# Kernel tuning notes

Measured on AMD Instinct MI355X. Metric: run time of the kernel, lower is better.

Reference implementation:

```python
import jax, jax.numpy as jnp
import numpy as np

B, S, D, H = 4, 1024, 1024, 16
HD = D // H  # head_dim = 64


def setup_inputs() -> dict:
    key = jax.random.key(0)
    ks = jax.random.split(key, 12)
    std = 1.0 / np.sqrt(D)
    inp = {
        "query": jax.random.normal(ks[0], (B, S, D), jnp.float32),
        "key": jax.random.normal(ks[1], (B, S, D), jnp.float32),
        "value": jax.random.normal(ks[2], (B, S, D), jnp.float32),
        # four Linear(embed_dim, embed_dim) layers: q, k, v, out
        "Wq": jax.random.normal(ks[3], (D, D), jnp.float32) * std,
        "bq": jnp.zeros((D,), jnp.float32),
        "Wk": jax.random.normal(ks[4], (D, D), jnp.float32) * std,
        "bk": jnp.zeros((D,), jnp.float32),
        "Wv": jax.random.normal(ks[5], (D, D), jnp.float32) * std,
        "bv": jnp.zeros((D,), jnp.float32),
        "Wo": jax.random.normal(ks[6], (D, D), jnp.float32) * std,
        "bo": jnp.zeros((D,), jnp.float32),
        # compressor: Linear(num_heads, 1)
        "Wc": jax.random.normal(ks[7], (H,), jnp.float32) / np.sqrt(H),
        "bc": jnp.zeros((), jnp.float32),
    }
    return inp


def reference(query, key, value, Wq, bq, Wk, bk, Wv, bv, Wo, bo, Wc, bc):
    b, s, d = query.shape
    h, hd = H, HD

    def proj(x, W, bias):
        # [b,s,d] @ [d,d] -> [b,h,s,hd]
        y = jnp.einsum('bsd,de->bse', x, W) + bias
        return y.reshape(b, s, h, hd).transpose(0, 2, 1, 3)

    q = proj(query, Wq, bq)
    k = proj(key, Wk, bk)
    v = proj(value, Wv, bv)

    scores = jnp.einsum('bhqd,bhkd->bhqk', q, k) / np.sqrt(hd)
    p_attn = jax.nn.softmax(scores, axis=-1)  # [b,h,s,s]; dropout is identity in eval

    x = jnp.einsum('bhqk,bhkd->bhqd', p_attn, v)
    x = x.transpose(0, 2, 1, 3).reshape(b, s, d)
    out = jnp.einsum('bsd,de->bse', x, Wo) + bo

    # head compression: Linear(num_heads, 1) over head axis -> [b,1,s,s]
    attn_c = (jnp.einsum('bhqk,h->bqk', p_attn, Wc) + bc)[:, None, :, :]
    return out, attn_c
```

## Files before the change

### kernel.cpp

```cpp
#include <hip/hip_runtime.h>
#include <hip/hip_bf16.h>

#define SS 1024
#define DD 1024
#define HH 16
#define HDh 64

typedef short bf16x8 __attribute__((ext_vector_type(8)));
typedef float f32x4 __attribute__((ext_vector_type(4)));

__device__ inline unsigned short f2bf(float f) {
    union { __hip_bfloat16 h; unsigned short u; } cv;
    cv.h = __float2bfloat16(f);
    return cv.u;
}
__device__ inline float bf2f(short u) {
    unsigned int x = ((unsigned int)(unsigned short)u) << 16;
    return __uint_as_float(x);
}

#define PIN4(a, b, c, d) asm volatile("" : "+v"(a), "+v"(b), "+v"(c), "+v"(d))

__device__ inline void gload_lds16(const unsigned short* g, unsigned short* l) {
    __builtin_amdgcn_global_load_lds(
        (const __attribute__((address_space(1))) unsigned int*)g,
        (__attribute__((address_space(3))) unsigned int*)l, 16, 0, 0);
}

__global__ __launch_bounds__(256) void prep(
    const float* __restrict__ a, const float* __restrict__ b, const float* __restrict__ c,
    unsigned short* __restrict__ oa, unsigned short* __restrict__ ob, unsigned short* __restrict__ oc,
    const float* __restrict__ Wq, const float* __restrict__ Wk,
    const float* __restrict__ Wv, const float* __restrict__ Wo,
    unsigned short* __restrict__ oq, unsigned short* __restrict__ okk,
    unsigned short* __restrict__ ov, unsigned short* __restrict__ oo)
{
    __shared__ float tile[32][33];
    int bid = blockIdx.x;
    if (bid < 4096) {
        size_t i = ((size_t)bid * 256 + threadIdx.x) * 4;
        float4 va = *(const float4*)(a + i);
        float4 vb = *(const float4*)(b + i);
        float4 vc = *(const float4*)(c + i);
        *(ushort4*)(oa + i) = make_ushort4(f2bf(va.x), f2bf(va.y), f2bf(va.z), f2bf(va.w));
        *(ushort4*)(ob + i) = make_ushort4(f2bf(vb.x), f2bf(vb.y), f2bf(vb.z), f2bf(vb.w));
        *(ushort4*)(oc + i) = make_ushort4(f2bf(vc.x), f2bf(vc.y), f2bf(vc.z), f2bf(vc.w));
    } else {
        int idx = bid - 4096;
        int z = idx >> 10;
        const float* W = z == 0 ? Wq : (z == 1 ? Wk : (z == 2 ? Wv : Wo));
        unsigned short* O = z == 0 ? oq : (z == 1 ? okk : (z == 2 ? ov : oo));
        int e0 = (idx & 31) * 32, d0 = ((idx >> 5) & 31) * 32;
        int r = threadIdx.x >> 3, c4 = (threadIdx.x & 7) * 4;
        float4 v = *(const float4*)(W + (size_t)(d0 + r) * DD + e0 + c4);
        tile[r][c4 + 0] = v.x; tile[r][c4 + 1] = v.y; tile[r][c4 + 2] = v.z; tile[r][c4 + 3] = v.w;
        __syncthreads();
        ushort4 u = make_ushort4(f2bf(tile[c4 + 0][r]), f2bf(tile[c4 + 1][r]),
                                 f2bf(tile[c4 + 2][r]), f2bf(tile[c4 + 3][r]));
        *(ushort4*)(O + (size_t)(e0 + r) * DD + d0 + c4) = u;
    }
}

template<int BK>
__device__ inline void gemm128_core(const unsigned short* __restrict__ A,
                                    const unsigned short* __restrict__ Bt,
                                    const float* __restrict__ bias,
                                    void* __restrict__ out, int mode, float oscale,
                                    int m0, int n0)
{
    __shared__ unsigned short As[128 * BK];
    __shared__ unsigned short Bs[128 * BK];
    int t = threadIdx.x;
    int w = t >> 6, lane = t & 63, quad = lane >> 4, l15 = lane & 15;
    int wm = w >> 1, wn = w & 1;

    f32x4 zero = {0.f, 0.f, 0.f, 0.f};
    f32x4 acc[4][4];
#pragma unroll
    for (int i = 0; i < 4; i++)
#pragma unroll
        for (int j = 0; j < 4; j++) acc[i][j] = zero;

    for (int k0 = 0; k0 < DD; k0 += BK) {
        __syncthreads();
        if constexpr (BK == 32) {
#pragma unroll
            for (int i = 0; i < 4; i++) {
                int chunk = w + i * 4;
                int half = chunk >> 3;
                int c = chunk & 7;
                const unsigned short* g = (half ? Bt : A)
                    + (size_t)((half ? n0 : m0) + c * 16 + (lane >> 2)) * DD + k0 + (lane & 3) * 8;
                unsigned short* l = (half ? Bs : As) + c * 512 + lane * 8;
                gload_lds16(g, l);
            }
        } else {
#pragma unroll
            for (int i = 0; i < 8; i++) {
                int chunk = w + i * 4;
                int half = chunk >> 4;
                int sub = chunk & 15;
                const unsigned short* g = (half ? Bt : A)
                    + (size_t)((half ? n0 : m0) + (sub >> 1) * 16 + (lane >> 2)) * DD
                    + k0 + (sub & 1) * 32 + (lane & 3) * 8;
                unsigned short* l = (half ? Bs : As) + sub * 512 + lane * 8;
                gload_lds16(g, l);
            }
        }
        __syncthreads();
        if constexpr (BK == 32) {
            bf16x8 af[4], bfr[4];
#pragma unroll
            for (int mi = 0; mi < 4; mi++)
                af[mi] = *(const bf16x8*)&As[(wm * 64 + mi * 16 + l15) * 32 + quad * 8];
#pragma unroll
            for (int ni = 0; ni < 4; ni++)
                bfr[ni] = *(const bf16x8*)&Bs[(wn * 64 + ni * 16 + l15) * 32 + quad * 8];
#pragma unroll
            for (int mi = 0; mi < 4; mi++)
#pragma unroll
                for (int ni = 0; ni < 4; ni++)
                    acc[mi][ni] = __builtin_amdgcn_mfma_f32_16x16x32_bf16(af[mi], bfr[ni], acc[mi][ni], 0, 0, 0);
        } else {
#pragma unroll
            for (int kk = 0; kk < 2; kk++) {
                bf16x8 af[4], bfr[4];
#pragma unroll
                for (int mi = 0; mi < 4; mi++)
                    af[mi] = *(const bf16x8*)&As[((wm * 4 + mi) * 2 + kk) * 512 + l15 * 32 + quad * 8];
#pragma unroll
                for (int ni = 0; ni < 4; ni++)
                    bfr[ni] = *(const bf16x8*)&Bs[((wn * 4 + ni) * 2 + kk) * 512 + l15 * 32 + quad * 8];
#pragma unroll
                for (int mi = 0; mi < 4; mi++)
#pragma unroll
                    for (int ni = 0; ni < 4; ni++)
                        acc[mi][ni] = __builtin_amdgcn_mfma_f32_16x16x32_bf16(af[mi], bfr[ni], acc[mi][ni], 0, 0, 0);
            }
        }
    }

#pragma unroll
    for (int mi = 0; mi < 4; mi++)
#pragma unroll
        for (int ni = 0; ni < 4; ni++) {
            int n = n0 + wn * 64 + ni * 16 + l15;
            float bv = bias[n];
#pragma unroll
            for (int r = 0; r < 4; r++) {
                int m = m0 + wm * 64 + mi * 16 + quad * 4 + r;
                float v = (acc[mi][ni][r] + bv) * oscale;
                if (mode == 2) {
                    ((float*)out)[(size_t)m * DD + n] = v;
                } else {
                    int bb = m >> 10, s = m & 1023, hh = n >> 6, d = n & 63;
                    size_t head = (size_t)(bb * HH + hh) << 16;
                    size_t off;
                    if (mode == 0) {
                        off = head + (((size_t)(s >> 4) * 2 + (d >> 5)) * 64
                              + ((d >> 3) & 3) * 16 + (s & 15)) * 8 + (d & 7);
                    } else {
                        off = head + (((size_t)(s >> 5) * 4 + (d >> 4)) * 64
                              + ((s >> 3) & 3) * 16 + (d & 15)) * 8 + (s & 7);
                    }
                    ((unsigned short*)out)[off] = f2bf(v);
                }
            }
        }
}

#define SCLQ 0.18033688f

__global__ __launch_bounds__(256, 3) void gemm_qkv(
    const unsigned short* __restrict__ xq, const unsigned short* __restrict__ xk,
    const unsigned short* __restrict__ xv,
    const unsigned short* __restrict__ wtq, const unsigned short* __restrict__ wtk,
    const unsigned short* __restrict__ wtv,
    const float* __restrict__ bq, const float* __restrict__ bk, const float* __restrict__ bv,
    unsigned short* __restrict__ q, unsigned short* __restrict__ k, unsigned short* __restrict__ v)
{
    int bid = blockIdx.x;
    int swz = (bid & 7) * 96 + (bid >> 3);
    int z = swz >> 8, rem = swz & 255;
    int n0 = (rem & 7) * 128, m0 = (rem >> 3) * 128;
    const unsigned short* A  = z == 0 ? xq  : (z == 1 ? xk  : xv);
    const unsigned short* Bt = z == 0 ? wtq : (z == 1 ? wtk : wtv);
    const float* bias        = z == 0 ? bq  : (z == 1 ? bk  : bv);
    void* out                = z == 0 ? (void*)q : (z == 1 ? (void*)k : (void*)v);
    gemm128_core<64>(A, Bt, bias, out, z == 2 ? 1 : 0, z == 0 ? SCLQ : 1.0f, m0, n0);
}

__global__ __launch_bounds__(256, 3) void gemm_o(
    const unsigned short* __restrict__ x, const unsigned short* __restrict__ wto,
    const float* __restrict__ bo, float* __restrict__ out)
{
    int bid = blockIdx.x;
    int swz = (bid & 7) * 32 + (bid >> 3);
    int n0 = (swz & 7) * 128, m0 = (swz >> 3) * 128;
    gemm128_core<32>(x, wto, bo, out, 2, 1.0f, m0, n0);
}


__global__ __launch_bounds__(512, 4) void fattn_kernel(
    const unsigned short* __restrict__ qf, const unsigned short* __restrict__ kf,
    const unsigned short* __restrict__ vf, float* __restrict__ Z,
    unsigned short* __restrict__ xat)
{
    __shared__ __align__(16) unsigned short kls[2][2048];
    __shared__ __align__(16) unsigned short vls[2][2048];
    __shared__ __align__(16) unsigned short plds[8][640];
    int t = threadIdx.x, w = t >> 6, lane = t & 63, quad = lane >> 4, l15 = lane & 15;
    int bid = blockIdx.x;
    int swz = (bid & 7) * 64 + (bid >> 3);
    int bh = swz >> 3, m0 = (swz & 7) * 128;
    int b = bh >> 4, h = bh & 15;
    const unsigned short* qh = qf + ((size_t)bh << 16);
    const unsigned short* kh = kf + ((size_t)bh << 16);
    const unsigned short* vh = vf + ((size_t)bh << 16);

    bf16x8 qfrag[2];
    int s16b = (m0 >> 4) + w;
#pragma unroll
    for (int dh = 0; dh < 2; dh++)
        qfrag[dh] = *(const bf16x8*)(qh + (size_t)(s16b * 2 + dh) * 512 + lane * 8);

    f32x4 zero = {0.f, 0.f, 0.f, 0.f};
    f32x4 oacc[4];
#pragma unroll
    for (int ni = 0; ni < 4; ni++) oacc[ni] = zero;
    float zacc = 0.f;

    const unsigned short* ssrc = (w < 4 ? kh + (size_t)w * 512
                                        : vh + (size_t)(w - 4) * 512) + lane * 8;
    int sinner = (w < 4 ? w * 512 : (w - 4) * 512) + lane * 8;

    gload_lds16(ssrc, (w < 4 ? kls[0] : vls[0]) + sinner);
    __syncthreads();

    int cur = 0;
    for (int kt = 0; kt < 32; kt++) {
        if (kt < 31)
            gload_lds16(ssrc + (size_t)(kt + 1) * 2048,
                        (w < 4 ? kls[cur ^ 1] : vls[cur ^ 1]) + sinner);

        bf16x8 kc[4], vc[4];
#pragma unroll
        for (int i = 0; i < 4; i++) {
            kc[i] = *(const bf16x8*)&kls[cur][i * 512 + lane * 8];
            vc[i] = *(const bf16x8*)&vls[cur][i * 512 + lane * 8];
        }

        f32x4 st[2];
#pragma unroll
        for (int si = 0; si < 2; si++) {
            st[si] = __builtin_amdgcn_mfma_f32_16x16x32_bf16(kc[si * 2 + 0], qfrag[0], zero, 0, 0, 0);
            st[si] = __builtin_amdgcn_mfma_f32_16x16x32_bf16(kc[si * 2 + 1], qfrag[1], st[si], 0, 0, 0);
        }

#pragma unroll
        for (int si = 0; si < 2; si++) {
            float p0 = exp2f(st[si][0]);
            float p1 = exp2f(st[si][1]);
            float p2 = exp2f(st[si][2]);
            float p3 = exp2f(st[si][3]);
            zacc += (p0 + p1) + (p2 + p3);
            unsigned int pk0 = (unsigned int)f2bf(p0) | ((unsigned int)f2bf(p1) << 16);
            unsigned int pk1 = (unsigned int)f2bf(p2) | ((unsigned int)f2bf(p3) << 16);
            *(uint2*)&plds[w][l15 * 40 + si * 16 + quad * 4] = make_uint2(pk0, pk1);
        }
        bf16x8 pa = *(const bf16x8*)&plds[w][l15 * 40 + quad * 8];

#pragma unroll
        for (int ni = 0; ni < 4; ni++)
            oacc[ni] = __builtin_amdgcn_mfma_f32_16x16x32_bf16(pa, vc[ni], oacc[ni], 0, 0, 0);

        __syncthreads();
        cur ^= 1;
    }

    float zt = zacc;
    zt += __shfl_xor(zt, 16);
    zt += __shfl_xor(zt, 32);
    if (quad == 0)
        Z[(size_t)bh * 1024 + m0 + w * 16 + l15] = zt;

#pragma unroll
    for (int r = 0; r < 4; r++) {
        int qrow = quad * 4 + r;
        float iz = 1.f / __shfl(zt, qrow);
        int q = m0 + w * 16 + qrow;
#pragma unroll
        for (int ni = 0; ni < 4; ni++)
            xat[((size_t)(b * 1024 + q)) * 1024 + h * 64 + ni * 16 + l15] =
                f2bf(oacc[ni][r] * iz);
    }
}

__global__ __launch_bounds__(256, 3) void tail_kernel(
    const unsigned short* __restrict__ qf, const unsigned short* __restrict__ kf,
    const float* __restrict__ Z, const float* __restrict__ Wc,
    const float* __restrict__ bcp, float* __restrict__ attc,
    const unsigned short* __restrict__ xat, const unsigned short* __restrict__ wto,
    const float* __restrict__ bo, float* __restrict__ out0)
{
    if (blockIdx.x >= 512) {
        int bid2 = blockIdx.x - 512;
        int swz = (bid2 & 7) * 32 + (bid2 >> 3);
        int n0 = (swz & 7) * 128, m0 = (swz >> 3) * 128;
        gemm128_core<32>(xat, wto, bo, out0, 2, 1.0f, m0, n0);
        return;
    }
    __shared__ unsigned short ks[2][8192];
    int t = threadIdx.x, w = t >> 6, lane = t & 63, quad = lane >> 4, l15 = lane & 15;
    int bid = blockIdx.x;
    int u = (bid & 7) * 64 + (bid >> 3);
    int kb = u & 7, qg = (u >> 3) & 15, b = u >> 7;
    int qt = qg * 4 + w;
    int q = qt * 16 + l15;
    float bc = *bcp;
    f32x4 zero = {0.f, 0.f, 0.f, 0.f};
    f32x4 acc[4][2];
#pragma unroll
    for (int kt = 0; kt < 4; kt++)
#pragma unroll
        for (int si = 0; si < 2; si++) acc[kt][si] = zero;

    float wzv[16];
#pragma unroll
    for (int h = 0; h < 16; h++)
        wzv[h] = Wc[h] / Z[(size_t)(b * 16 + h) * 1024 + q];

    {
        const unsigned short* src = kf + ((size_t)(b * 16) << 16) + (size_t)(kb * 16) * 512;
#pragma unroll
        for (int i = 0; i < 4; i++) {
            int c = w + i * 4;
            gload_lds16(src + (size_t)c * 512 + lane * 8, ks[0] + c * 512 + lane * 8);
        }
    }
    __syncthreads();

    int cb = 0;
    for (int h = 0; h < 16; h++) {
        int bh = b * 16 + h;
        const unsigned short* qh = qf + ((size_t)bh << 16);
        bf16x8 qfr0 = *(const bf16x8*)(qh + (size_t)(qt * 2 + 0) * 512 + lane * 8);
        bf16x8 qfr1 = *(const bf16x8*)(qh + (size_t)(qt * 2 + 1) * 512 + lane * 8);
        if (h < 15) {
            const unsigned short* src = kf + ((size_t)(bh + 1) << 16) + (size_t)(kb * 16) * 512;
#pragma unroll
            for (int i = 0; i < 4; i++) {
                int c = w + i * 4;
                gload_lds16(src + (size_t)c * 512 + lane * 8, ks[cb ^ 1] + c * 512 + lane * 8);
            }
        }
        float wz = wzv[h];
#pragma unroll
        for (int kt = 0; kt < 4; kt++) {
            bf16x8 kfr[4];
#pragma unroll
            for (int i = 0; i < 4; i++)
                kfr[i] = *(const bf16x8*)&ks[cb][(size_t)(kt * 4 + i) * 512 + lane * 8];
#pragma unroll
            for (int si = 0; si < 2; si++) {
                f32x4 st = __builtin_amdgcn_mfma_f32_16x16x32_bf16(kfr[si * 2 + 0], qfr0, zero, 0, 0, 0);
                st = __builtin_amdgcn_mfma_f32_16x16x32_bf16(kfr[si * 2 + 1], qfr1, st, 0, 0, 0);
#pragma unroll
                for (int r = 0; r < 4; r++)
                    acc[kt][si][r] += wz * exp2f(st[r]);
            }
        }
        __syncthreads();
        cb ^= 1;
    }
#pragma unroll
    for (int kt = 0; kt < 4; kt++)
#pragma unroll
        for (int si = 0; si < 2; si++) {
            float4 vv = make_float4(acc[kt][si][0] + bc, acc[kt][si][1] + bc,
                                    acc[kt][si][2] + bc, acc[kt][si][3] + bc);
            *(float4*)(attc + ((size_t)(b * 1024 + q)) * 1024 + kb * 128 + kt * 32 + si * 16 + quad * 4) = vv;
        }
}

#define LDK(f) (*(const bf16x8*)(kh + ((size_t)(f) * 64 + lane) * 8))
#define LDV(f) (*(const bf16x8*)(vh + ((size_t)(f) * 64 + lane) * 8))

__global__ __launch_bounds__(1024, 4) void attn_kernel(
    const unsigned short* __restrict__ qf, const unsigned short* __restrict__ kf,
    const unsigned short* __restrict__ vf, const float* __restrict__ Wc,
    const float* __restrict__ bcp, unsigned short* __restrict__ xout,
    float* __restrict__ attc)
{
    __shared__ float accc[16][1028];
    __shared__ unsigned short tsc[16][16][36];

    int t = threadIdx.x, w = t >> 6, lane = t & 63, quad = lane >> 4, l15 = lane & 15;
    int b = blockIdx.x >> 6, qt = blockIdx.x & 63;
    int h = w;

    for (int i = t; i < 16 * 1028; i += 1024) (&accc[0][0])[i] = 0.f;
    __syncthreads();

    const unsigned short* qh = qf + ((size_t)(b * HH + h) << 16);
    const unsigned short* kh = kf + ((size_t)(b * HH + h) << 16);
    const unsigned short* vh = vf + ((size_t)(b * HH + h) << 16);
    float wc = Wc[h], bc = *bcp;
    f32x4 zero = {0.f, 0.f, 0.f, 0.f};

    bf16x8 a0 = *(const bf16x8*)(qh + ((size_t)(qt * 2 + 0) * 64 + lane) * 8);
    bf16x8 a1 = *(const bf16x8*)(qh + ((size_t)(qt * 2 + 1) * 64 + lane) * 8);

    float rs[4] = {0.f, 0.f, 0.f, 0.f};
    bf16x8 c0 = LDK(0), c1 = LDK(1), c2 = LDK(2), c3 = LDK(3);
    PIN4(c0, c1, c2, c3);
    bf16x8 d0 = LDK(4), d1 = LDK(5), d2 = LDK(6), d3 = LDK(7);
    PIN4(d0, d1, d2, d3);
#pragma unroll 2
    for (int g = 0; g < 32; g++) {
        int gn = g < 30 ? g + 2 : 31;
        bf16x8 n0 = LDK(gn * 4 + 0), n1 = LDK(gn * 4 + 1);
        bf16x8 n2 = LDK(gn * 4 + 2), n3 = LDK(gn * 4 + 3);
        PIN4(n0, n1, n2, n3);
        f32x4 s0 = zero, s1 = zero;
        s0 = __builtin_amdgcn_mfma_f32_16x16x32_bf16(a0, c0, s0, 0, 0, 0);
        s0 = __builtin_amdgcn_mfma_f32_16x16x32_bf16(a1, c1, s0, 0, 0, 0);
        s1 = __builtin_amdgcn_mfma_f32_16x16x32_bf16(a0, c2, s1, 0, 0, 0);
        s1 = __builtin_amdgcn_mfma_f32_16x16x32_bf16(a1, c3, s1, 0, 0, 0);
#pragma unroll
        for (int r = 0; r < 4; r++) rs[r] += exp2f(s0[r]) + exp2f(s1[r]);
        c0 = d0; c1 = d1; c2 = d2; c3 = d3;
        d0 = n0; d1 = n1; d2 = n2; d3 = n3;
    }
#pragma unroll
    for (int r = 0; r < 4; r++) {
        rs[r] += __shfl_xor(rs[r], 1);
        rs[r] += __shfl_xor(rs[r], 2);
        rs[r] += __shfl_xor(rs[r], 4);
        rs[r] += __shfl_xor(rs[r], 8);
    }
    float invC[4], sC[4];
#pragma unroll
    for (int r = 0; r < 4; r++) { invC[r] = 1.f / rs[r]; sC[r] = wc * invC[r]; }

    f32x4 o0 = zero, o1 = zero, o2 = zero, o3 = zero;
    int cc0 = (2 * w) & 31;
    bf16x8 k0 = LDK(cc0 * 4 + 0), k1 = LDK(cc0 * 4 + 1);
    bf16x8 k2 = LDK(cc0 * 4 + 2), k3 = LDK(cc0 * 4 + 3);
    PIN4(k0, k1, k2, k3);
    bf16x8 v0 = LDV(cc0 * 4 + 0), v1 = LDV(cc0 * 4 + 1);
    bf16x8 v2 = LDV(cc0 * 4 + 2), v3 = LDV(cc0 * 4 + 3);
    PIN4(v0, v1, v2, v3);
#pragma unroll 2
    for (int i = 0; i < 32; i++) {
        int cc = (i + 2 * w) & 31;
        int cn = ((i + 1) + 2 * w) & 31;
        bf16x8 kn0 = LDK(cn * 4 + 0), kn1 = LDK(cn * 4 + 1);
        bf16x8 kn2 = LDK(cn * 4 + 2), kn3 = LDK(cn * 4 + 3);
        PIN4(kn0, kn1, kn2, kn3);
        bf16x8 vn0 = LDV(cn * 4 + 0), vn1 = LDV(cn * 4 + 1);
        bf16x8 vn2 = LDV(cn * 4 + 2), vn3 = LDV(cn * 4 + 3);
        PIN4(vn0, vn1, vn2, vn3);

        f32x4 s0 = zero, s1 = zero;
        s0 = __builtin_amdgcn_mfma_f32_16x16x32_bf16(a0, k0, s0, 0, 0, 0);
        s0 = __builtin_amdgcn_mfma_f32_16x16x32_bf16(a1, k1, s0, 0, 0, 0);
        s1 = __builtin_amdgcn_mfma_f32_16x16x32_bf16(a0, k2, s1, 0, 0, 0);
        s1 = __builtin_amdgcn_mfma_f32_16x16x32_bf16(a1, k3, s1, 0, 0, 0);

#pragma unroll
        for (int r = 0; r < 4; r++) {
            float p0 = exp2f(s0[r]);
            float p1 = exp2f(s1[r]);
            int row = quad * 4 + r;
            tsc[w][row][l15] = f2bf(p0);
            tsc[w][row][16 + l15] = f2bf(p1);
            atomicAdd(&accc[row][cc * 32 + l15], sC[r] * p0);
            atomicAdd(&accc[row][cc * 32 + 16 + l15], sC[r] * p1);
        }
        bf16x8 ap = *(const bf16x8*)&tsc[w][l15][quad * 8];

        o0 = __builtin_amdgcn_mfma_f32_16x16x32_bf16(ap, v0, o0, 0, 0, 0);
        o1 = __builtin_amdgcn_mfma_f32_16x16x32_bf16(ap, v1, o1, 0, 0, 0);
        o2 = __builtin_amdgcn_mfma_f32_16x16x32_bf16(ap, v2, o2, 0, 0, 0);
        o3 = __builtin_amdgcn_mfma_f32_16x16x32_bf16(ap, v3, o3, 0, 0, 0);
        k0 = kn0; k1 = kn1; k2 = kn2; k3 = kn3;
        v0 = vn0; v1 = vn1; v2 = vn2; v3 = vn3;
    }

    f32x4 oo[4] = {o0, o1, o2, o3};
#pragma unroll
    for (int j = 0; j < 4; j++)
#pragma unroll
        for (int r = 0; r < 4; r++) {
            int row = quad * 4 + r;
            xout[((size_t)(b * SS) + qt * 16 + row) * DD + h * 64 + j * 16 + l15] =
                f2bf(oo[j][r] * invC[r]);
        }

    __syncthreads();
    for (int i = t; i < 16 * 1024; i += 1024) {
        int row = i >> 10, col = i & 1023;
        attc[((size_t)b * SS + qt * 16 + row) * SS + col] = accc[row][col] + bc;
    }
}

extern "C" void kernel_launch(void* const* d_in, const int* in_sizes, int n_in,
                              void* d_out, int out_size, void* d_ws, size_t ws_size,
                              hipStream_t stream) {
    const float* query = (const float*)d_in[0];
    const float* key   = (const float*)d_in[1];
    const float* value = (const float*)d_in[2];
    const float* Wq = (const float*)d_in[3];
    const float* bq = (const float*)d_in[4];
    const float* Wk = (const float*)d_in[5];
    const float* bk = (const float*)d_in[6];
    const float* Wv = (const float*)d_in[7];
    const float* bv = (const float*)d_in[8];
    const float* Wo = (const float*)d_in[9];
    const float* bo = (const float*)d_in[10];
    const float* Wc = (const float*)d_in[11];
    const float* bc = (const float*)d_in[12];

    unsigned short* ws  = (unsigned short*)d_ws;
    unsigned short* xq  = ws;
    unsigned short* xk  = xq  + (size_t)4194304;
    unsigned short* xv  = xk  + (size_t)4194304;
    unsigned short* wtq = xv  + (size_t)4194304;
    unsigned short* wtk = wtq + (size_t)1048576;
    unsigned short* wtv = wtk + (size_t)1048576;
    unsigned short* wto = wtv + (size_t)1048576;
    unsigned short* qfb = wto + (size_t)1048576;
    unsigned short* kfb = qfb + (size_t)4194304;
    unsigned short* vfb = kfb + (size_t)4194304;
    unsigned short* xat = vfb + (size_t)4194304;

    float* out0 = (float*)d_out;
    float* attc = out0 + (size_t)4194304;

    const size_t base_bytes = 67108864;
    const size_t z_bytes = 262144;
    bool fast = ws_size >= base_bytes + z_bytes;

    hipLaunchKernelGGL(prep, dim3(8192), dim3(256), 0, stream,
                       query, key, value, xq, xk, xv,
                       Wq, Wk, Wv, Wo, wtq, wtk, wtv, wto);
    hipLaunchKernelGGL(gemm_qkv, dim3(768), dim3(256), 0, stream,
                       xq, xk, xv, wtq, wtk, wtv, bq, bk, bv, qfb, kfb, vfb);

    if (fast) {
        float* Zbuf = (float*)((char*)d_ws + base_bytes);
        hipLaunchKernelGGL(fattn_kernel, dim3(512), dim3(512), 0, stream,
                           qfb, kfb, vfb, Zbuf, xat);
        hipLaunchKernelGGL(tail_kernel, dim3(768), dim3(256), 0, stream,
                           qfb, kfb, Zbuf, Wc, bc, attc,
                           xat, wto, bo, out0);
    } else {
        hipLaunchKernelGGL(attn_kernel, dim3(256), dim3(1024), 0, stream,
                           qfb, kfb, vfb, Wc, bc, xat, attc);
        hipLaunchKernelGGL(gemm_o, dim3(256), dim3(256), 0, stream,
                           xat, wto, bo, out0);
    }
}
```

Before: 225.3 us.

## Double attention K/V tile depth, share LDS pool, use BK=64 for output GEMM

The flash-attention kernel now stages 64 keys per pipeline step instead of 32, so every wave loads both K and V chunks and two sub-tiles are processed per barrier, halving loop iterations and syncs. The GEMM core now takes caller-provided LDS buffers, and the tail kernel shares one pool between its compression path and its fused output-projection GEMM, which now runs with BK=64. The aim is to cut barrier and loop overhead and LDS over-allocation in the fused tail kernel. The cost is more LDS per attention block, which may lower occupancy.

```diff
diff --git a/kernel.cpp b/kernel.cpp
--- a/kernel.cpp
+++ b/kernel.cpp
@@ -62,14 +62,13 @@
 }
 
 template<int BK>
-__device__ inline void gemm128_core(const unsigned short* __restrict__ A,
+__device__ inline void gemm128_core(unsigned short* As, unsigned short* Bs,
+                                    const unsigned short* __restrict__ A,
                                     const unsigned short* __restrict__ Bt,
                                     const float* __restrict__ bias,
                                     void* __restrict__ out, int mode, float oscale,
                                     int m0, int n0)
 {
-    __shared__ unsigned short As[128 * BK];
-    __shared__ unsigned short Bs[128 * BK];
     int t = threadIdx.x;
     int w = t >> 6, lane = t & 63, quad = lane >> 4, l15 = lane & 15;
     int wm = w >> 1, wn = w & 1;
@@ -179,6 +178,7 @@
     const float* __restrict__ bq, const float* __restrict__ bk, const float* __restrict__ bv,
     unsigned short* __restrict__ q, unsigned short* __restrict__ k, unsigned short* __restrict__ v)
 {
+    __shared__ unsigned short pool[16384];
     int bid = blockIdx.x;
     int swz = (bid & 7) * 96 + (bid >> 3);
     int z = swz >> 8, rem = swz & 255;
@@ -187,17 +187,19 @@
     const unsigned short* Bt = z == 0 ? wtq : (z == 1 ? wtk : wtv);
     const float* bias        = z == 0 ? bq  : (z == 1 ? bk  : bv);
     void* out                = z == 0 ? (void*)q : (z == 1 ? (void*)k : (void*)v);
-    gemm128_core<64>(A, Bt, bias, out, z == 2 ? 1 : 0, z == 0 ? SCLQ : 1.0f, m0, n0);
+    gemm128_core<64>(pool, pool + 8192, A, Bt, bias, out, z == 2 ? 1 : 0,
+                     z == 0 ? SCLQ : 1.0f, m0, n0);
 }
 
 __global__ __launch_bounds__(256, 3) void gemm_o(
     const unsigned short* __restrict__ x, const unsigned short* __restrict__ wto,
     const float* __restrict__ bo, float* __restrict__ out)
 {
+    __shared__ unsigned short pool[16384];
     int bid = blockIdx.x;
     int swz = (bid & 7) * 32 + (bid >> 3);
     int n0 = (swz & 7) * 128, m0 = (swz >> 3) * 128;
-    gemm128_core<32>(x, wto, bo, out, 2, 1.0f, m0, n0);
+    gemm128_core<64>(pool, pool + 8192, x, wto, bo, out, 2, 1.0f, m0, n0);
 }
 
 
@@ -206,8 +208,8 @@
     const unsigned short* __restrict__ vf, float* __restrict__ Z,
     unsigned short* __restrict__ xat)
 {
-    __shared__ __align__(16) unsigned short kls[2][2048];
-    __shared__ __align__(16) unsigned short vls[2][2048];
+    __shared__ __align__(16) unsigned short kls[2][4096];
+    __shared__ __align__(16) unsigned short vls[2][4096];
     __shared__ __align__(16) unsigned short plds[8][640];
     int t = threadIdx.x, w = t >> 6, lane = t & 63, quad = lane >> 4, l15 = lane & 15;
     int bid = blockIdx.x;
@@ -230,49 +232,54 @@
     for (int ni = 0; ni < 4; ni++) oacc[ni] = zero;
     float zacc = 0.f;
 
-    const unsigned short* ssrc = (w < 4 ? kh + (size_t)w * 512
-                                        : vh + (size_t)(w - 4) * 512) + lane * 8;
-    int sinner = (w < 4 ? w * 512 : (w - 4) * 512) + lane * 8;
-
-    gload_lds16(ssrc, (w < 4 ? kls[0] : vls[0]) + sinner);
+    const unsigned short* ksrc = kh + (size_t)w * 512 + lane * 8;
+    const unsigned short* vsrc = vh + (size_t)w * 512 + lane * 8;
+    int koff = w * 512 + lane * 8;
+
+    gload_lds16(ksrc, kls[0] + koff);
+    gload_lds16(vsrc, vls[0] + koff);
     __syncthreads();
 
     int cur = 0;
-    for (int kt = 0; kt < 32; kt++) {
-        if (kt < 31)
-            gload_lds16(ssrc + (size_t)(kt + 1) * 2048,
-                        (w < 4 ? kls[cur ^ 1] : vls[cur ^ 1]) + sinner);
-
-        bf16x8 kc[4], vc[4];
-#pragma unroll
-        for (int i = 0; i < 4; i++) {
-            kc[i] = *(const bf16x8*)&kls[cur][i * 512 + lane * 8];
-            vc[i] = *(const bf16x8*)&vls[cur][i * 512 + lane * 8];
-        }
-
-        f32x4 st[2];
-#pragma unroll
-        for (int si = 0; si < 2; si++) {
-            st[si] = __builtin_amdgcn_mfma_f32_16x16x32_bf16(kc[si * 2 + 0], qfrag[0], zero, 0, 0, 0);
-            st[si] = __builtin_amdgcn_mfma_f32_16x16x32_bf16(kc[si * 2 + 1], qfrag[1], st[si], 0, 0, 0);
-        }
-
-#pragma unroll
-        for (int si = 0; si < 2; si++) {
-            float p0 = exp2f(st[si][0]);
-            float p1 = exp2f(st[si][1]);
-            float p2 = exp2f(st[si][2]);
-            float p3 = exp2f(st[si][3]);
-            zacc += (p0 + p1) + (p2 + p3);
-            unsigned int pk0 = (unsigned int)f2bf(p0) | ((unsigned int)f2bf(p1) << 16);
-            unsigned int pk1 = (unsigned int)f2bf(p2) | ((unsigned int)f2bf(p3) << 16);
-            *(uint2*)&plds[w][l15 * 40 + si * 16 + quad * 4] = make_uint2(pk0, pk1);
-        }
-        bf16x8 pa = *(const bf16x8*)&plds[w][l15 * 40 + quad * 8];
-
-#pragma unroll
-        for (int ni = 0; ni < 4; ni++)
-            oacc[ni] = __builtin_amdgcn_mfma_f32_16x16x32_bf16(pa, vc[ni], oacc[ni], 0, 0, 0);
+    for (int p = 0; p < 16; p++) {
+        if (p < 15) {
+            gload_lds16(ksrc + (size_t)(p + 1) * 4096, kls[cur ^ 1] + koff);
+            gload_lds16(vsrc + (size_t)(p + 1) * 4096, vls[cur ^ 1] + koff);
+        }
+
+#pragma unroll
+        for (int sub = 0; sub < 2; sub++) {
+            bf16x8 kc[4], vc[4];
+#pragma unroll
+            for (int i = 0; i < 4; i++) {
+                kc[i] = *(const bf16x8*)&kls[cur][(sub * 4 + i) * 512 + lane * 8];
+                vc[i] = *(const bf16x8*)&vls[cur][(sub * 4 + i) * 512 + lane * 8];
+            }
+
+            f32x4 st[2];
+#pragma unroll
+            for (int si = 0; si < 2; si++) {
+                st[si] = __builtin_amdgcn_mfma_f32_16x16x32_bf16(kc[si * 2 + 0], qfrag[0], zero, 0, 0, 0);
+                st[si] = __builtin_amdgcn_mfma_f32_16x16x32_bf16(kc[si * 2 + 1], qfrag[1], st[si], 0, 0, 0);
+            }
+
+#pragma unroll
+            for (int si = 0; si < 2; si++) {
+                float p0 = exp2f(st[si][0]);
+                float p1 = exp2f(st[si][1]);
+                float p2 = exp2f(st[si][2]);
+                float p3 = exp2f(st[si][3]);
+                zacc += (p0 + p1) + (p2 + p3);
+                unsigned int pk0 = (unsigned int)f2bf(p0) | ((unsigned int)f2bf(p1) << 16);
+                unsigned int pk1 = (unsigned int)f2bf(p2) | ((unsigned int)f2bf(p3) << 16);
+                *(uint2*)&plds[w][l15 * 40 + si * 16 + quad * 4] = make_uint2(pk0, pk1);
+            }
+            bf16x8 pa = *(const bf16x8*)&plds[w][l15 * 40 + quad * 8];
+
+#pragma unroll
+            for (int ni = 0; ni < 4; ni++)
+                oacc[ni] = __builtin_amdgcn_mfma_f32_16x16x32_bf16(pa, vc[ni], oacc[ni], 0, 0, 0);
+        }
 
         __syncthreads();
         cur ^= 1;
@@ -303,14 +310,16 @@
     const unsigned short* __restrict__ xat, const unsigned short* __restrict__ wto,
     const float* __restrict__ bo, float* __restrict__ out0)
 {
+    __shared__ __align__(16) unsigned short pool[16384];
     if (blockIdx.x >= 512) {
         int bid2 = blockIdx.x - 512;
         int swz = (bid2 & 7) * 32 + (bid2 >> 3);
         int n0 = (swz & 7) * 128, m0 = (swz >> 3) * 128;
-        gemm128_core<32>(xat, wto, bo, out0, 2, 1.0f, m0, n0);
+        gemm128_core<64>(pool, pool + 8192, xat, wto, bo, out0, 2, 1.0f, m0, n0);
         return;
     }
-    __shared__ unsigned short ks[2][8192];
+    unsigned short* ks0 = pool;
+    unsigned short* ks1 = pool + 8192;
     int t = threadIdx.x, w = t >> 6, lane = t & 63, quad = lane >> 4, l15 = lane & 15;
     int bid = blockIdx.x;
     int u = (bid & 7) * 64 + (bid >> 3);
@@ -335,7 +344,7 @@
 #pragma unroll
         for (int i = 0; i < 4; i++) {
             int c = w + i * 4;
-            gload_lds16(src + (size_t)c * 512 + lane * 8, ks[0] + c * 512 + lane * 8);
+            gload_lds16(src + (size_t)c * 512 + lane * 8, ks0 + c * 512 + lane * 8);
         }
     }
     __syncthreads();
@@ -348,19 +357,21 @@
         bf16x8 qfr1 = *(const bf16x8*)(qh + (size_t)(qt * 2 + 1) * 512 + lane * 8);
         if (h < 15) {
             const unsigned short* src = kf + ((size_t)(bh + 1) << 16) + (size_t)(kb * 16) * 512;
+            unsigned short* dst = (cb ? ks0 : ks1);
 #pragma unroll
             for (int i = 0; i < 4; i++) {
                 int c = w + i * 4;
-                gload_lds16(src + (size_t)c * 512 + lane * 8, ks[cb ^ 1] + c * 512 + lane * 8);
-            }
-        }
+                gload_lds16(src + (size_t)c * 512 + lane * 8, dst + c * 512 + lane * 8);
+            }
+        }
+        const unsigned short* cbuf = (cb ? ks1 : ks0);
         float wz = wzv[h];
 #pragma unroll
         for (int kt = 0; kt < 4; kt++) {
             bf16x8 kfr[4];
 #pragma unroll
             for (int i = 0; i < 4; i++)
-                kfr[i] = *(const bf16x8*)&ks[cb][(size_t)(kt * 4 + i) * 512 + lane * 8];
+                kfr[i] = *(const bf16x8*)&cbuf[(size_t)(kt * 4 + i) * 512 + lane * 8];
 #pragma unroll
             for (int si = 0; si < 2; si++) {
                 f32x4 st = __builtin_amdgcn_mfma_f32_16x16x32_bf16(kfr[si * 2 + 0], qfr0, zero, 0, 0, 0);
```

Measured after the change: 240.0 us. +6.5%, slower.
